# Optimization experiments

Hardware: AMD Instinct MI355X
Metric: run time of the kernel (lower is better)

The kernel has to match this reference:

```python
import jax, jax.numpy as jnp
import numpy as np

B, N, D, H, R, K = 64, 197, 768, 3072, 16, 1


def setup_inputs() -> dict:
    key = jax.random.key(0)
    ks = jax.random.split(key, 9)
    s1 = 1.0 / np.sqrt(D)
    s2 = 1.0 / np.sqrt(H)
    return {
        "x": jax.random.normal(ks[0], (B, N, D), dtype=jnp.float32),
        "W1": jax.random.normal(ks[1], (H, D), dtype=jnp.float32) * s1,
        "b1": jax.random.normal(ks[2], (H,), dtype=jnp.float32) * s1,
        "A1": jax.random.normal(ks[3], (K, R, D), dtype=jnp.float32) * s1,
        "B1": jax.random.normal(ks[4], (K, H, R), dtype=jnp.float32) * 0.01,
        "W2": jax.random.normal(ks[5], (D, H), dtype=jnp.float32) * s2,
        "b2": jax.random.normal(ks[6], (D,), dtype=jnp.float32) * s2,
        "A2": jax.random.normal(ks[7], (K, R, H), dtype=jnp.float32) * s2,
        "B2": jax.random.normal(ks[8], (K, D, R), dtype=jnp.float32) * 0.01,
    }


def _lora(x, A, Bm):
    # result of torch: (B @ (A @ x^T.unsqueeze(1))).sum(1).transpose(1,2)
    # A: [K, r, d_in], Bm: [K, d_out, r], x: [b, n, d_in] -> [b, n, d_out]
    t = jnp.einsum('krd,bnd->bknr', A, x)          # low-rank projection
    return jnp.einsum('kor,bknr->bno', Bm, t)      # expand + sum over K


def reference(x, W1, b1, A1, B1, W2, b2, A2, B2):
    # fc1 (Linear + LoRA correction)
    h = jnp.einsum('bnd,hd->bnh', x, W1) + b1 + _lora(x, A1, B1)
    # exact (erf-based) GELU, matching torch nn.GELU default
    h = jax.nn.gelu(h, approximate=False)
    # dropout p=0 and norm=Identity by default -> no-ops
    out = jnp.einsum('bnh,dh->bnd', h, W2) + b2 + _lora(h, A2, B2)
    return out
```

## Files before the change

kernel.cpp:

```cpp
#include <hip/hip_runtime.h>
#include <math.h>

#define M_ROWS 12608
#define D_DIM  768
#define H_DIM  3072

typedef __bf16 bf16_t;
typedef __bf16 bf16x8 __attribute__((ext_vector_type(8)));
typedef float  f32x4  __attribute__((ext_vector_type(4)));

__device__ __forceinline__ float gelu_fast(float v) {
  float v2 = v * v;
  float z = v * fmaf(0.044715f, v2, 1.0f);
  float e = __expf(-1.5957691216057308f * z);
  return v * __builtin_amdgcn_rcpf(1.0f + e);
}

__device__ __forceinline__ void gld16(const bf16_t* g, char* l) {
  __builtin_amdgcn_global_load_lds(
      (const __attribute__((address_space(1))) void*)g,
      (__attribute__((address_space(3))) void*)l, 16, 0, 0);
}

#define CAST_BLOCKS 9456
#define FOLD_BLOCKS 9216

__device__ __forceinline__ void fold_body(const float* __restrict__ W,
                                          const float* __restrict__ A,
                                          const float* __restrict__ Bm,
                                          bf16_t* __restrict__ Weff,
                                          int IN, long idx) {
  int o = (int)(idx / IN);
  int i = (int)(idx - (long)o * IN);
  float s = W[idx];
#pragma unroll
  for (int r = 0; r < 16; ++r)
    s += Bm[o * 16 + r] * A[r * IN + i];
  Weff[idx] = (bf16_t)s;
}

__global__ __launch_bounds__(256) void prep_kernel(
    const float* __restrict__ x, bf16_t* __restrict__ xb,
    const float* __restrict__ W1, const float* __restrict__ A1,
    const float* __restrict__ B1, bf16_t* __restrict__ W1eff,
    const float* __restrict__ W2, const float* __restrict__ A2,
    const float* __restrict__ B2, bf16_t* __restrict__ W2eff) {
  const int b = blockIdx.x;
  if (b < CAST_BLOCKS) {
    long i = ((long)b * 256 + threadIdx.x) * 4;
    float4 v = *(const float4*)(x + i);
    xb[i + 0] = (bf16_t)v.x; xb[i + 1] = (bf16_t)v.y;
    xb[i + 2] = (bf16_t)v.z; xb[i + 3] = (bf16_t)v.w;
  } else if (b < CAST_BLOCKS + FOLD_BLOCKS) {
    long idx = (long)(b - CAST_BLOCKS) * 256 + threadIdx.x;
    fold_body(W1, A1, B1, W1eff, D_DIM, idx);
  } else {
    long idx = (long)(b - CAST_BLOCKS - FOLD_BLOCKS) * 256 + threadIdx.x;
    fold_body(W2, A2, B2, W2eff, H_DIM, idx);
  }
}

__global__ __launch_bounds__(256, 4) void gemm1_kernel(
    const bf16_t* __restrict__ Amat, const bf16_t* __restrict__ Bmat,
    const float* __restrict__ bias, bf16_t* __restrict__ Cmat,
    int Mrows, int Ncols, int Kd) {
  __shared__ char smem[32768];
  bf16_t* lds = (bf16_t*)smem;
  float* sT = (float*)smem;

  const int xcd = blockIdx.x & 7, t = blockIdx.x >> 3;
  const int colb = t / 13;
  const int rowb = (t % 13) * 8 + xcd;
  if (rowb >= 99) return;
  const int row0 = rowb * 128, col0 = colb * 128;

  const int tid = threadIdx.x, lane = tid & 63, wave = tid >> 6;
  const int wm = wave & 1, wn = wave >> 1;

  const bf16_t* gA[4]; const bf16_t* gB[4];
  int ldsA[4], ldsB[4];
#pragma unroll
  for (int q = 0; q < 4; ++q) {
    int c = tid + q * 256;
    int r = c >> 3, kkg = (c & 7) ^ (r & 7);
    int ra = row0 + r; if (ra > Mrows - 1) ra = Mrows - 1;
    gA[q] = Amat + (size_t)ra * Kd + kkg * 8;
    gB[q] = Bmat + (size_t)(col0 + r) * Kd + kkg * 8;
    ldsA[q] = c * 16;
    ldsB[q] = 16384 + c * 16;
  }

  const int rl = lane & 15, kc = lane >> 4;
  int aoffs[4], boffs[4];
#pragma unroll
  for (int i = 0; i < 4; ++i) {
    int ra = wm * 64 + i * 16 + rl;
    int rb = wn * 64 + i * 16 + rl;
    aoffs[i] = ra * 64 + ((kc ^ (ra & 7)) * 8);
    boffs[i] = 8192 + rb * 64 + ((kc ^ (rb & 7)) * 8);
  }

  f32x4 acc[4][4] = {};
  const int iters = Kd / 64;

#pragma unroll
  for (int q = 0; q < 4; ++q) {
    gld16(gA[q], smem + ldsA[q]);
    gld16(gB[q], smem + ldsB[q]);
    gA[q] += 64; gB[q] += 64;
  }
  __syncthreads();

  for (int it = 0; it < iters; ++it) {
#pragma unroll
    for (int ks = 0; ks < 2; ++ks) {
      bf16x8 af[4], bfr[4];
#pragma unroll
      for (int i = 0; i < 4; ++i) af[i] = *(const bf16x8*)(lds + (aoffs[i] ^ (ks * 32)));
#pragma unroll
      for (int i = 0; i < 4; ++i) bfr[i] = *(const bf16x8*)(lds + (boffs[i] ^ (ks * 32)));
#pragma unroll
      for (int mi = 0; mi < 4; ++mi)
#pragma unroll
        for (int ni = 0; ni < 4; ++ni)
          acc[mi][ni] = __builtin_amdgcn_mfma_f32_16x16x32_bf16(
              af[mi], bfr[ni], acc[mi][ni], 0, 0, 0);
    }
    if (it + 1 < iters) {
      __syncthreads();
#pragma unroll
      for (int q = 0; q < 4; ++q) {
        gld16(gA[q], smem + ldsA[q]);
        gld16(gB[q], smem + ldsB[q]);
        gA[q] += 64; gB[q] += 64;
      }
      __syncthreads();
    }
  }

  const int crow = (lane >> 4) * 4, ccol = lane & 15;
  __syncthreads();
#pragma unroll
  for (int p = 0; p < 2; ++p) {
#pragma unroll
    for (int s = 0; s < 2; ++s) {
      int mi = 2 * p + s;
#pragma unroll
      for (int ni = 0; ni < 4; ++ni)
#pragma unroll
        for (int r = 0; r < 4; ++r) {
          int rr = wm * 32 + s * 16 + crow + r;
          sT[rr * 128 + ((wn * 64 + ni * 16 + ccol) ^ ((rr & 7) << 2))] =
              acc[mi][ni][r];
        }
    }
    __syncthreads();
    const int erow = tid >> 2, eseg = tid & 3;
    const int grow = row0 + (erow >> 5) * 64 + (2 * p + ((erow >> 4) & 1)) * 16 + (erow & 15);
    if (grow < Mrows) {
      const float* srow = sT + erow * 128;
      const float* bsrc = bias + col0 + eseg * 32;
      const int v = (erow & 7) << 2;
      bf16_t ov[32];
#pragma unroll
      for (int a = 0; a < 8; ++a) {
        const f32x4 q4 = *(const f32x4*)(srow + (((eseg * 32) + a * 4) ^ v));
#pragma unroll
        for (int b = 0; b < 4; ++b)
          ov[a * 4 + b] = (bf16_t)gelu_fast(q4[b] + bsrc[a * 4 + b]);
      }
      bf16_t* dst = (bf16_t*)Cmat + (size_t)grow * Ncols + col0 + eseg * 32;
#pragma unroll
      for (int k = 0; k < 4; ++k)
        *(bf16x8*)(dst + k * 8) = *(bf16x8*)(ov + k * 8);
    }
    __syncthreads();
  }
}

__global__ __launch_bounds__(256, 3) void gemm2_kernel(
    const bf16_t* __restrict__ Amat, const bf16_t* __restrict__ Bmat,
    const float* __restrict__ bias, float* __restrict__ Cmat,
    int Mrows, int Ncols, int Kd) {
  __shared__ char smem[49152];
  bf16_t* lds = (bf16_t*)smem;

  const int xcd = blockIdx.x & 7, t = blockIdx.x >> 3;
  const int rowb = (t / 3) * 4 + (xcd & 3);
  if (rowb >= 197) return;
  const int colb = (xcd >> 2) * 3 + (t % 3);
  const int row0 = rowb * 64, col0 = colb * 128;

  const int tid = threadIdx.x, lane = tid & 63, wave = tid >> 6;
  const int wm = wave & 1, wn = wave >> 1;

  const bf16_t* gA[4]; int ldsA[4];
  const bf16_t* gB[8]; int ldsB[8];
#pragma unroll
  for (int q = 0; q < 4; ++q) {
    int c = tid + q * 256;
    int r = c >> 4, kkg = (c & 15) ^ (r & 7);
    gA[q] = Amat + (size_t)(row0 + r) * Kd + kkg * 8;
    ldsA[q] = c * 16;
  }
#pragma unroll
  for (int q = 0; q < 8; ++q) {
    int c = tid + q * 256;
    int r = c >> 4, kkg = (c & 15) ^ (r & 7);
    gB[q] = Bmat + (size_t)(col0 + r) * Kd + kkg * 8;
    ldsB[q] = 16384 + c * 16;
  }

  const int rl = lane & 15, kc = lane >> 4;
  int aoffs[2], boffs[4];
#pragma unroll
  for (int i = 0; i < 2; ++i) {
    int ra = wm * 32 + i * 16 + rl;
    aoffs[i] = ra * 128 + ((kc ^ (ra & 7)) * 8);
  }
#pragma unroll
  for (int i = 0; i < 4; ++i) {
    int rb = wn * 64 + i * 16 + rl;
    boffs[i] = 8192 + rb * 128 + ((kc ^ (rb & 7)) * 8);
  }

  f32x4 acc[2][4] = {};
  const int iters = Kd / 128;

#pragma unroll
  for (int q = 0; q < 4; ++q) { gld16(gA[q], smem + ldsA[q]); gA[q] += 128; }
#pragma unroll
  for (int q = 0; q < 8; ++q) { gld16(gB[q], smem + ldsB[q]); gB[q] += 128; }
  __syncthreads();

  for (int it = 0; it < iters; ++it) {
#pragma unroll
    for (int ks = 0; ks < 4; ++ks) {
      bf16x8 af[2], bfr[4];
#pragma unroll
      for (int i = 0; i < 2; ++i) af[i] = *(const bf16x8*)(lds + (aoffs[i] ^ (ks * 32)));
#pragma unroll
      for (int i = 0; i < 4; ++i) bfr[i] = *(const bf16x8*)(lds + (boffs[i] ^ (ks * 32)));
#pragma unroll
      for (int mi = 0; mi < 2; ++mi)
#pragma unroll
        for (int ni = 0; ni < 4; ++ni)
          acc[mi][ni] = __builtin_amdgcn_mfma_f32_16x16x32_bf16(
              af[mi], bfr[ni], acc[mi][ni], 0, 0, 0);
    }
    if (it + 1 < iters) {
      __syncthreads();
#pragma unroll
      for (int q = 0; q < 4; ++q) { gld16(gA[q], smem + ldsA[q]); gA[q] += 128; }
#pragma unroll
      for (int q = 0; q < 8; ++q) { gld16(gB[q], smem + ldsB[q]); gB[q] += 128; }
      __syncthreads();
    }
  }

  const int crow = (lane >> 4) * 4, ccol = lane & 15;
#pragma unroll
  for (int ni = 0; ni < 4; ++ni) {
    const int gc = col0 + wn * 64 + ni * 16 + ccol;
    const float bv = bias[gc];
#pragma unroll
    for (int mi = 0; mi < 2; ++mi) {
      const int gr = row0 + wm * 32 + mi * 16 + crow;
#pragma unroll
      for (int r = 0; r < 4; ++r)
        Cmat[(size_t)(gr + r) * Ncols + gc] = acc[mi][ni][r] + bv;
    }
  }
}

extern "C" void kernel_launch(void* const* d_in, const int* in_sizes, int n_in,
                              void* d_out, int out_size, void* d_ws, size_t ws_size,
                              hipStream_t stream) {
  const float* x  = (const float*)d_in[0];
  const float* W1 = (const float*)d_in[1];
  const float* b1 = (const float*)d_in[2];
  const float* A1 = (const float*)d_in[3];
  const float* B1 = (const float*)d_in[4];
  const float* W2 = (const float*)d_in[5];
  const float* b2 = (const float*)d_in[6];
  const float* A2 = (const float*)d_in[7];
  const float* B2 = (const float*)d_in[8];
  float* out = (float*)d_out;

  char* ws = (char*)d_ws;
  bf16_t* xb    = (bf16_t*)ws;
  bf16_t* W1eff = (bf16_t*)(ws + 19366144);
  bf16_t* W2eff = (bf16_t*)(ws + 19366144 + 4718592);
  bf16_t* hbuf  = (bf16_t*)(ws + 19366144 + 2 * 4718592);

  prep_kernel<<<CAST_BLOCKS + 2 * FOLD_BLOCKS, 256, 0, stream>>>(
      x, xb, W1, A1, B1, W1eff, W2, A2, B2, W2eff);

  gemm1_kernel<<<2496, 256, 0, stream>>>(
      xb, W1eff, b1, hbuf, M_ROWS, H_DIM, D_DIM);
  gemm2_kernel<<<1200, 256, 0, stream>>>(
      hbuf, W2eff, b2, out, M_ROWS, D_DIM, H_DIM);
}
```

Before: 283.9 us.

## Rewrite gemm1 as 256x256 tile, 8-wave, double-buffered LDS pipeline

New measurement: 311.1 us. +9.6%, slower.

```diff
diff --git a/kernel.cpp b/kernel.cpp
--- a/kernel.cpp
+++ b/kernel.cpp
@@ -60,119 +60,151 @@
   }
 }
 
-__global__ __launch_bounds__(256, 4) void gemm1_kernel(
+__global__ __launch_bounds__(512, 2) void gemm1_kernel(
     const bf16_t* __restrict__ Amat, const bf16_t* __restrict__ Bmat,
     const float* __restrict__ bias, bf16_t* __restrict__ Cmat,
     int Mrows, int Ncols, int Kd) {
-  __shared__ char smem[32768];
+  __shared__ char smem[131072];
   bf16_t* lds = (bf16_t*)smem;
   float* sT = (float*)smem;
 
-  const int xcd = blockIdx.x & 7, t = blockIdx.x >> 3;
-  const int colb = t / 13;
-  const int rowb = (t % 13) * 8 + xcd;
-  if (rowb >= 99) return;
-  const int row0 = rowb * 128, col0 = colb * 128;
+  const int colb = blockIdx.x / 50, rowb = blockIdx.x % 50;
+  const int row0 = rowb * 256, col0 = colb * 256;
 
   const int tid = threadIdx.x, lane = tid & 63, wave = tid >> 6;
   const int wm = wave & 1, wn = wave >> 1;
 
-  const bf16_t* gA[4]; const bf16_t* gB[4];
-  int ldsA[4], ldsB[4];
-#pragma unroll
-  for (int q = 0; q < 4; ++q) {
-    int c = tid + q * 256;
+  const bf16_t* gA[2][2]; const bf16_t* gB[2][2];
+  int ldsc[2];
+#pragma unroll
+  for (int q = 0; q < 2; ++q) {
+    int c = tid + q * 512;
     int r = c >> 3, kkg = (c & 7) ^ (r & 7);
-    int ra = row0 + r; if (ra > Mrows - 1) ra = Mrows - 1;
-    gA[q] = Amat + (size_t)ra * Kd + kkg * 8;
-    gB[q] = Bmat + (size_t)(col0 + r) * Kd + kkg * 8;
-    ldsA[q] = c * 16;
-    ldsB[q] = 16384 + c * 16;
+    ldsc[q] = c * 16;
+#pragma unroll
+    for (int h = 0; h < 2; ++h) {
+      int ra = row0 + h * 128 + r; if (ra > Mrows - 1) ra = Mrows - 1;
+      gA[h][q] = Amat + (size_t)ra * Kd + kkg * 8;
+      gB[h][q] = Bmat + (size_t)(col0 + h * 128 + r) * Kd + kkg * 8;
+    }
   }
 
   const int rl = lane & 15, kc = lane >> 4;
-  int aoffs[4], boffs[4];
+  const int abase0 = wm * 8192;
+  const int bbase0 = 16384 + (wn >> 1) * 8192;
+  int aoffs[2][4], boffs[4];
+#pragma unroll
+  for (int mq = 0; mq < 2; ++mq)
+#pragma unroll
+    for (int i = 0; i < 4; ++i) {
+      int rh = mq * 64 + i * 16 + rl;
+      aoffs[mq][i] = rh * 64 + ((kc ^ (rh & 7)) * 8);
+    }
 #pragma unroll
   for (int i = 0; i < 4; ++i) {
-    int ra = wm * 64 + i * 16 + rl;
-    int rb = wn * 64 + i * 16 + rl;
-    aoffs[i] = ra * 64 + ((kc ^ (ra & 7)) * 8);
-    boffs[i] = 8192 + rb * 64 + ((kc ^ (rb & 7)) * 8);
-  }
-
-  f32x4 acc[4][4] = {};
-  const int iters = Kd / 64;
-
-#pragma unroll
-  for (int q = 0; q < 4; ++q) {
-    gld16(gA[q], smem + ldsA[q]);
-    gld16(gB[q], smem + ldsB[q]);
-    gA[q] += 64; gB[q] += 64;
-  }
+    int rbl = (wn & 1) * 64 + i * 16 + rl;
+    boffs[i] = rbl * 64 + ((kc ^ (rbl & 7)) * 8);
+  }
+
+  f32x4 acc[8][4] = {};
+  const int NT = Kd / 64;
+
+  gld16(gB[0][0], smem + 32768 + ldsc[0]); gld16(gB[0][1], smem + 32768 + ldsc[1]);
+  gld16(gB[1][0], smem + 49152 + ldsc[0]); gld16(gB[1][1], smem + 49152 + ldsc[1]);
+  gld16(gA[0][0], smem +     0 + ldsc[0]); gld16(gA[1][0], smem + 16384 + ldsc[0]);
+  gld16(gA[0][1], smem +     0 + ldsc[1]); gld16(gA[1][1], smem + 16384 + ldsc[1]);
+#pragma unroll
+  for (int h = 0; h < 2; ++h)
+#pragma unroll
+    for (int q = 0; q < 2; ++q) { gA[h][q] += 64; gB[h][q] += 64; }
+  asm volatile("s_waitcnt vmcnt(2)" ::: "memory");
+  __builtin_amdgcn_sched_barrier(0);
+  __builtin_amdgcn_s_barrier();
+
+  for (int t = 0; t < NT; ++t) {
+    const bool st = (t + 1 < NT);
+    const int cb = (t & 1) * 32768;
+    const int sb = ((t + 1) & 1) * 65536;
+    bf16x8 bf[4][2];
+#pragma unroll
+    for (int p = 0; p < 4; ++p) {
+      const int mq = p >> 1, ks = p & 1;
+      bf16x8 af[4];
+#pragma unroll
+      for (int i = 0; i < 4; ++i)
+        af[i] = *(const bf16x8*)(lds + cb + abase0 + (aoffs[mq][i] ^ (ks * 32)));
+      if (p == 0) {
+#pragma unroll
+        for (int k2 = 0; k2 < 2; ++k2)
+#pragma unroll
+          for (int i = 0; i < 4; ++i)
+            bf[i][k2] = *(const bf16x8*)(lds + cb + bbase0 + (boffs[i] ^ (k2 * 32)));
+      }
+      if (st) {
+        if (p == 0)      { gld16(gB[0][0], smem+sb+32768+ldsc[0]); gld16(gB[0][1], smem+sb+32768+ldsc[1]); gB[0][0]+=64; gB[0][1]+=64; }
+        else if (p == 1) { gld16(gB[1][0], smem+sb+49152+ldsc[0]); gld16(gB[1][1], smem+sb+49152+ldsc[1]); gB[1][0]+=64; gB[1][1]+=64; }
+        else if (p == 2) { gld16(gA[0][0], smem+sb+    0+ldsc[0]); gld16(gA[1][0], smem+sb+16384+ldsc[0]); gA[0][0]+=64; gA[1][0]+=64; }
+        else             { gld16(gA[0][1], smem+sb+    0+ldsc[1]); gld16(gA[1][1], smem+sb+16384+ldsc[1]); gA[0][1]+=64; gA[1][1]+=64; }
+      }
+      __builtin_amdgcn_s_setprio(1);
+#pragma unroll
+      for (int i = 0; i < 4; ++i)
+#pragma unroll
+        for (int ni = 0; ni < 4; ++ni)
+          acc[mq * 4 + i][ni] = __builtin_amdgcn_mfma_f32_16x16x32_bf16(
+              af[i], bf[ni][ks], acc[mq * 4 + i][ni], 0, 0, 0);
+      __builtin_amdgcn_s_setprio(0);
+      if (p == 1) {
+        if (st) { asm volatile("s_waitcnt vmcnt(4)" ::: "memory"); }
+        else    { asm volatile("s_waitcnt vmcnt(0)" ::: "memory"); }
+        __builtin_amdgcn_sched_barrier(0);
+        __builtin_amdgcn_s_barrier();
+      } else if (p == 3 && st) {
+        asm volatile("s_waitcnt vmcnt(2)" ::: "memory");
+        __builtin_amdgcn_sched_barrier(0);
+        __builtin_amdgcn_s_barrier();
+      }
+    }
+  }
+
   __syncthreads();
-
-  for (int it = 0; it < iters; ++it) {
-#pragma unroll
-    for (int ks = 0; ks < 2; ++ks) {
-      bf16x8 af[4], bfr[4];
-#pragma unroll
-      for (int i = 0; i < 4; ++i) af[i] = *(const bf16x8*)(lds + (aoffs[i] ^ (ks * 32)));
-#pragma unroll
-      for (int i = 0; i < 4; ++i) bfr[i] = *(const bf16x8*)(lds + (boffs[i] ^ (ks * 32)));
-#pragma unroll
-      for (int mi = 0; mi < 4; ++mi)
+  const int crow = (lane >> 4) * 4, ccol = lane & 15;
+#pragma unroll
+  for (int P = 0; P < 4; ++P) {
+    if (wm == (P >> 1)) {
+      const int mq = P & 1;
+#pragma unroll
+      for (int i = 0; i < 4; ++i)
 #pragma unroll
         for (int ni = 0; ni < 4; ++ni)
-          acc[mi][ni] = __builtin_amdgcn_mfma_f32_16x16x32_bf16(
-              af[mi], bfr[ni], acc[mi][ni], 0, 0, 0);
-    }
-    if (it + 1 < iters) {
-      __syncthreads();
-#pragma unroll
-      for (int q = 0; q < 4; ++q) {
-        gld16(gA[q], smem + ldsA[q]);
-        gld16(gB[q], smem + ldsB[q]);
-        gA[q] += 64; gB[q] += 64;
+#pragma unroll
+          for (int r = 0; r < 4; ++r) {
+            int srow = i * 16 + crow + r;
+            int scol = wn * 64 + ni * 16 + ccol;
+            sT[srow * 256 + (scol ^ ((srow & 7) << 2))] = acc[mq * 4 + i][ni][r];
+          }
+    }
+    __syncthreads();
+    {
+      const int erow = tid >> 3, eseg = tid & 7;
+      const int grow = row0 + P * 64 + erow;
+      if (grow < Mrows) {
+        const float* srow_p = sT + erow * 256;
+        const float* bsrc = bias + col0 + eseg * 32;
+        const int v = (erow & 7) << 2;
+        bf16_t ov[32];
+#pragma unroll
+        for (int a = 0; a < 8; ++a) {
+          const f32x4 q4 = *(const f32x4*)(srow_p + ((eseg * 32 + a * 4) ^ v));
+#pragma unroll
+          for (int b = 0; b < 4; ++b)
+            ov[a * 4 + b] = (bf16_t)gelu_fast(q4[b] + bsrc[a * 4 + b]);
+        }
+        bf16_t* dst = Cmat + (size_t)grow * Ncols + col0 + eseg * 32;
+#pragma unroll
+        for (int k = 0; k < 4; ++k)
+          *(bf16x8*)(dst + k * 8) = *(bf16x8*)(ov + k * 8);
       }
-      __syncthreads();
-    }
-  }
-
-  const int crow = (lane >> 4) * 4, ccol = lane & 15;
-  __syncthreads();
-#pragma unroll
-  for (int p = 0; p < 2; ++p) {
-#pragma unroll
-    for (int s = 0; s < 2; ++s) {
-      int mi = 2 * p + s;
-#pragma unroll
-      for (int ni = 0; ni < 4; ++ni)
-#pragma unroll
-        for (int r = 0; r < 4; ++r) {
-          int rr = wm * 32 + s * 16 + crow + r;
-          sT[rr * 128 + ((wn * 64 + ni * 16 + ccol) ^ ((rr & 7) << 2))] =
-              acc[mi][ni][r];
-        }
-    }
-    __syncthreads();
-    const int erow = tid >> 2, eseg = tid & 3;
-    const int grow = row0 + (erow >> 5) * 64 + (2 * p + ((erow >> 4) & 1)) * 16 + (erow & 15);
-    if (grow < Mrows) {
-      const float* srow = sT + erow * 128;
-      const float* bsrc = bias + col0 + eseg * 32;
-      const int v = (erow & 7) << 2;
-      bf16_t ov[32];
-#pragma unroll
-      for (int a = 0; a < 8; ++a) {
-        const f32x4 q4 = *(const f32x4*)(srow + (((eseg * 32) + a * 4) ^ v));
-#pragma unroll
-        for (int b = 0; b < 4; ++b)
-          ov[a * 4 + b] = (bf16_t)gelu_fast(q4[b] + bsrc[a * 4 + b]);
-      }
-      bf16_t* dst = (bf16_t*)Cmat + (size_t)grow * Ncols + col0 + eseg * 32;
-#pragma unroll
-      for (int k = 0; k < 4; ++k)
-        *(bf16x8*)(dst + k * 8) = *(bf16x8*)(ov + k * 8);
     }
     __syncthreads();
   }
@@ -296,7 +328,7 @@
   prep_kernel<<<CAST_BLOCKS + 2 * FOLD_BLOCKS, 256, 0, stream>>>(
       x, xb, W1, A1, B1, W1eff, W2, A2, B2, W2eff);
 
-  gemm1_kernel<<<2496, 256, 0, stream>>>(
+  gemm1_kernel<<<600, 512, 0, stream>>>(
       xb, W1eff, b1, hbuf, M_ROWS, H_DIM, D_DIM);
   gemm2_kernel<<<1200, 256, 0, stream>>>(
       hbuf, W2eff, b2, out, M_ROWS, D_DIM, H_DIM);
```
